# Kernel optimization log

Hardware: AMD Instinct MI355X
Metric: run time of the kernel (lower is better)

## Reference

```python
import jax, jax.numpy as jnp
import numpy as np
from jax import lax

B, L, N = 64, 1024, 64
IN_SZ, MEM_SZ, DEC = 128, 1024, 3


def setup_inputs() -> dict:
    key = jax.random.key(0)
    ks = jax.random.split(key, 8)
    x = jax.random.normal(ks[0], (B, L, N), dtype=jnp.float32)
    # sensor net: Linear(N -> IN_SZ) with bias (stored as [in, out])
    W_sense = jax.random.normal(ks[1], (N, IN_SZ), dtype=jnp.float32) / np.sqrt(N)
    b_sense = jax.random.normal(ks[2], (IN_SZ,), dtype=jnp.float32) * 0.01
    # nBRC: ff_im Linear(IN_SZ -> 3*MEM_SZ, bias=False), ff_mm Linear(MEM_SZ -> 2*MEM_SZ, bias=False)
    W_im = jax.random.normal(ks[3], (IN_SZ, 3 * MEM_SZ), dtype=jnp.float32) / np.sqrt(IN_SZ)
    W_mm = jax.random.normal(ks[4], (MEM_SZ, 2 * MEM_SZ), dtype=jnp.float32) / np.sqrt(MEM_SZ)
    # actor net: Linear(MEM_SZ -> DEC) with bias
    W_act = jax.random.normal(ks[5], (MEM_SZ, DEC), dtype=jnp.float32) / np.sqrt(MEM_SZ)
    b_act = jax.random.normal(ks[6], (DEC,), dtype=jnp.float32) * 0.01
    return {"x": x, "W_sense": W_sense, "b_sense": b_sense,
            "W_im": W_im, "W_mm": W_mm, "W_act": W_act, "b_act": b_act}


def reference(x, W_sense, b_sense, W_im, W_mm, W_act, b_act):
    # sense: applied per-token (flattened in torch; equivalent broadcasted matmul)
    inputs = x @ W_sense + b_sense                      # [B, L, IN_SZ]
    # precompute the input projection for all timesteps in one GEMM
    proj = inputs @ W_im                                 # [B, L, 3*MEM_SZ]
    proj_t = jnp.moveaxis(proj, 1, 0)                    # [L, B, 3*MEM_SZ]
    h0 = jnp.zeros((x.shape[0], MEM_SZ), dtype=x.dtype)

    def step(h, p):
        i_a, i_c, i_o = jnp.split(p, 3, axis=-1)         # each [B, MEM_SZ]
        m = h @ W_mm                                      # [B, 2*MEM_SZ]
        m_a, m_c = jnp.split(m, 2, axis=-1)
        a = 1.0 + jnp.tanh(i_a + m_a)
        c = jax.nn.sigmoid(i_c + m_c)
        hn = c * h + (1.0 - c) * jnp.tanh(i_o + a * h)
        return hn, hn

    _, hs = lax.scan(step, h0, proj_t)                    # [L, B, MEM_SZ]
    memory = jnp.moveaxis(hs, 0, 1)                       # [B, L, MEM_SZ]
    logits = memory @ W_act + b_act                       # [B, L, DEC]
    return jax.nn.softmax(logits, axis=-1)
```

## Files before the change

### kernel.cpp

```cpp
#include <hip/hip_runtime.h>
#include <hip/hip_bf16.h>


#define B_TOT 64
#define L_SEQ 1024
#define N_IN 64
#define INSZ 128
#define MEM 1024
#define DEC 3

#define NGROUP 8
#define BG 8
#define NMEM 32
#define RING 16

typedef __hip_bfloat16 bf16;
typedef short bf16x8 __attribute__((ext_vector_type(8)));
typedef float f32x4 __attribute__((ext_vector_type(4)));
typedef int i32x4 __attribute__((ext_vector_type(4)));
typedef unsigned long long ull;

#define OFF_INPUTS 0
#define SZ_INPUTS  (L_SEQ * 64 * INSZ * 2)
#define OFF_WMM    (OFF_INPUTS + SZ_INPUTS)
#define SZ_WMM     (128 * 32 * 64 * 8 * 2)
#define OFF_WIM    (OFF_WMM + SZ_WMM)
#define SZ_WIM     (192 * 4 * 64 * 8 * 2)
#define OFF_HBUF   (OFF_WIM + SZ_WIM)
#define SZ_HBUF    (RING * NGROUP * BG * MEM * 2)
#define OFF_CTR    (OFF_HBUF + SZ_HBUF)
#define SZ_CTR     ((4096 + 256) * 4)

__device__ __forceinline__ float fast_tanh(float x) {
    float e = __expf(2.f * x);
    return 1.f - 2.f / (e + 1.f);
}
__device__ __forceinline__ float fast_sigmoid(float x) {
    return 1.f / (1.f + __expf(-x));
}

__global__ void k_sense(const float* __restrict__ x, const float* __restrict__ Ws,
                        const float* __restrict__ bs, bf16* __restrict__ inputs) {
    int t = blockIdx.x;
    int tid = threadIdx.x;
    __shared__ float xls[64][64];
    __shared__ float wls[64][128];
    for (int idx = tid; idx < 64 * 64; idx += 256) {
        int b = idx >> 6, k = idx & 63;
        xls[b][k] = x[((size_t)b * L_SEQ + t) * N_IN + k];
    }
    for (int idx = tid; idx < 64 * 128; idx += 256) {
        int k = idx >> 7, j = idx & 127;
        wls[k][j] = Ws[k * INSZ + j];
    }
    __syncthreads();
    int j = tid & 127;
    int bh = tid >> 7;
    float bj = bs[j];
    for (int bi = 0; bi < 32; ++bi) {
        int b = bh * 32 + bi;
        float acc = bj;
#pragma unroll
        for (int k = 0; k < 64; ++k) acc += xls[b][k] * wls[k][j];
        inputs[((size_t)t * 64 + b) * INSZ + j] = (bf16)acc;
    }
}

__global__ void k_pack(const float* __restrict__ Wmm, const float* __restrict__ Wim,
                       bf16* __restrict__ pmm, bf16* __restrict__ pim) {
    int idx = blockIdx.x * 256 + threadIdx.x;
    const int NMMF = 128 * 32 * 64 * 8;
    if (idx < NMMF) {
        int j = idx & 7, lane = (idx >> 3) & 63, kb = (idx >> 9) & 31, ct = idx >> 14;
        int n = ct * 16 + (lane & 15);
        int k = kb * 32 + ((lane >> 4) << 3) + j;
        pmm[idx] = (bf16)Wmm[(size_t)k * 2048 + n];
    } else {
        int idx2 = idx - NMMF;
        if (idx2 < 192 * 4 * 64 * 8) {
            int j = idx2 & 7, lane = (idx2 >> 3) & 63, kb = (idx2 >> 9) & 3, ct = idx2 >> 11;
            int n = ct * 16 + (lane & 15);
            int k = kb * 32 + ((lane >> 4) << 3) + j;
            pim[idx2] = (bf16)Wim[(size_t)k * 3072 + n];
        }
    }
}

__launch_bounds__(256, 1)
__global__ void k_main(const bf16* __restrict__ inputs, const bf16* __restrict__ pmm,
                       const bf16* __restrict__ pim, const float* __restrict__ Wact,
                       const float* __restrict__ bact, bf16* __restrict__ hbuf,
                       float* __restrict__ out, unsigned int* __restrict__ ctr) {
    const int g = blockIdx.x & 7;
    const int m = blockIdx.x >> 3;
    const int tid = (int)threadIdx.x;
    const int wave = tid >> 6;
    const int lane = tid & 63;
    const int r16 = lane & 15;
    const int q = lane >> 4;

    __shared__ float ilds[2][3][2][8][16];
    __shared__ float mpart[2][4][4][8][16];
    __shared__ float wact_lds[3072];
    __shared__ float aplds[2][4][3];
    __shared__ float bactl[3];
    __shared__ unsigned idsl[256];
    __shared__ int fflagl;
    __shared__ float outbuf[L_SEQ * 3];

    for (int idx = tid; idx < 3072; idx += 256) wact_lds[idx] = Wact[idx];
    if (tid < 3) bactl[tid] = bact[tid];

    bf16x8 wb[4][8];
    {
        int base_ct[4] = {2 * m, 2 * m + 1, 64 + 2 * m, 65 + 2 * m};
#pragma unroll
        for (int t4 = 0; t4 < 4; ++t4)
#pragma unroll
            for (int kk = 0; kk < 8; ++kk)
                wb[t4][kk] = *(const bf16x8*)(pmm +
                    (((size_t)base_ct[t4] * 32 + (wave * 8 + kk)) * 64 + lane) * 8);
    }
    bf16x8 wi[2][4];
    if (wave < 3) {
#pragma unroll
        for (int tl = 0; tl < 2; ++tl) {
            int ct2 = wave * 64 + m * 2 + tl;
#pragma unroll
            for (int kb2 = 0; kb2 < 4; ++kb2)
                wi[tl][kb2] = *(const bf16x8*)(pim + (((size_t)ct2 * 4 + kb2) * 64 + lane) * 8);
        }
    }

    f32x4 hreg = {0.f, 0.f, 0.f, 0.f};
    const int erow = lane >> 3;
    const int ec = lane & 7;
    const int ep = ec >> 2;
    const int ecl = (ec & 3) * 4;

    unsigned int* flags = ctr + g * 512;
    unsigned int* ids   = ctr + 4096;

    unsigned xid;
    asm volatile("s_getreg_b32 %0, hwreg(HW_REG_XCC_ID)" : "=s"(xid));
    if (tid == 0)
        __hip_atomic_store(&ids[g * 32 + m], xid + 1u, __ATOMIC_RELAXED,
                           __HIP_MEMORY_SCOPE_AGENT);
    if (wave == 0) {
        int sb = 1 << 20;
        unsigned v0 = 0, v1 = 0, v2 = 0, v3 = 0;
        bool all = false;
        while (!all && --sb > 0) {
            v0 = __hip_atomic_load(&ids[lane], __ATOMIC_RELAXED, __HIP_MEMORY_SCOPE_AGENT);
            v1 = __hip_atomic_load(&ids[64 + lane], __ATOMIC_RELAXED, __HIP_MEMORY_SCOPE_AGENT);
            v2 = __hip_atomic_load(&ids[128 + lane], __ATOMIC_RELAXED, __HIP_MEMORY_SCOPE_AGENT);
            v3 = __hip_atomic_load(&ids[192 + lane], __ATOMIC_RELAXED, __HIP_MEMORY_SCOPE_AGENT);
            all = (bool)__all((int)(v0 && v1 && v2 && v3));
        }
        idsl[lane] = v0; idsl[64 + lane] = v1; idsl[128 + lane] = v2; idsl[192 + lane] = v3;
    }
    __syncthreads();
    if (tid == 0) {
        int f = 1;
        for (int g2 = 0; g2 < 8; ++g2) {
            unsigned r = idsl[g2 * 32];
            for (int k2 = 1; k2 < 32; ++k2) f &= (idsl[g2 * 32 + k2] == r);
        }
        fflagl = f;
    }
    __syncthreads();
    const bool fastf = (fflagl != 0);

    bf16x8 afin[4];
    auto load_in = [&](int t) {
        if (wave < 3) {
            int brow = g * 8 + (r16 & 7);
            const bf16* src = inputs + ((size_t)t * 64 + brow) * INSZ + q * 8;
#pragma unroll
            for (int kb2 = 0; kb2 < 4; ++kb2)
                afin[kb2] = *(const bf16x8*)(src + kb2 * 32);
        }
    };
    auto mma_in_deposit = [&](int t) {
        if (wave < 3) {
            f32x4 a0 = (f32x4){0.f, 0.f, 0.f, 0.f};
            f32x4 a1 = (f32x4){0.f, 0.f, 0.f, 0.f};
#pragma unroll
            for (int kb2 = 0; kb2 < 4; ++kb2) {
                a0 = __builtin_amdgcn_mfma_f32_16x16x32_bf16(afin[kb2], wi[0][kb2], a0, 0, 0, 0);
                a1 = __builtin_amdgcn_mfma_f32_16x16x32_bf16(afin[kb2], wi[1][kb2], a1, 0, 0, 0);
            }
            if (q < 2) {
#pragma unroll
                for (int reg = 0; reg < 4; ++reg) {
                    ilds[t & 1][wave][0][q * 4 + reg][r16] = a0[reg];
                    ilds[t & 1][wave][1][q * 4 + reg][r16] = a1[reg];
                }
            }
        }
    };

    auto poll_own = [&](unsigned target) {
        int k = wave * 8 + (lane & 7);
        bool act = lane < 8;
        unsigned vbest = act ? 0u : target;
        int rounds = 0;
        int sb = 1 << 18;
        while (--sb > 0) {
            if (act && vbest < target) {
                unsigned vm = __hip_atomic_load(&flags[k * 16], __ATOMIC_RELAXED,
                                                __HIP_MEMORY_SCOPE_AGENT);
                if (vm > vbest) vbest = vm;
            }
            if (__all((int)(vbest >= target))) break;
            if (++rounds > 8) __builtin_amdgcn_s_sleep(1);
        }
    };

    auto hload = [&](int t_src, int gg) -> ushort4 {
        int c0 = gg * 4;
        const bf16* hp = hbuf +
            ((size_t)(((t_src & (RING - 1)) * NGROUP + g)) * (BG * MEM)) +
            (c0 >> 5) * 256 + m * 32 + (c0 & 31);
        return *(const ushort4*)hp;
    };
    auto emit_accum = [&](ushort4 hv, int gg, float& p0, float& p1, float& p2) {
        int c0 = gg * 4;
        float h0 = __uint_as_float((unsigned)hv.x << 16);
        float h1 = __uint_as_float((unsigned)hv.y << 16);
        float h2 = __uint_as_float((unsigned)hv.z << 16);
        float h3 = __uint_as_float((unsigned)hv.w << 16);
        const f32x4* wp = (const f32x4*)&wact_lds[c0 * 3];
        f32x4 w0 = wp[0], w1 = wp[1], w2 = wp[2];
        p0 += h0 * w0[0] + h1 * w0[3] + h2 * w1[2] + h3 * w2[1];
        p1 += h0 * w0[1] + h1 * w1[0] + h2 * w1[3] + h3 * w2[2];
        p2 += h0 * w0[2] + h1 * w1[1] + h2 * w2[0] + h3 * w2[3];
    };
    auto emit_reduce = [&](int t_src, float p0, float p1, float p2) {
#pragma unroll
        for (int off = 32; off >= 1; off >>= 1) {
            p0 += __shfl_xor(p0, off);
            p1 += __shfl_xor(p1, off);
            p2 += __shfl_xor(p2, off);
        }
        if (lane == 0) {
            aplds[t_src & 1][wave][0] = p0;
            aplds[t_src & 1][wave][1] = p1;
            aplds[t_src & 1][wave][2] = p2;
        }
    };
    auto fin = [&](int tout) {
        int pr = tout & 1;
        float l0 = aplds[pr][0][0] + aplds[pr][1][0] + aplds[pr][2][0] + bactl[0];
        float l1 = aplds[pr][0][1] + aplds[pr][1][1] + aplds[pr][2][1] + bactl[1];
        float l2 = aplds[pr][0][2] + aplds[pr][1][2] + aplds[pr][2][2] + bactl[2];
        float mx = fmaxf(l0, fmaxf(l1, l2));
        float e0 = __expf(l0 - mx), e1 = __expf(l1 - mx), e2 = __expf(l2 - mx);
        float inv = 1.f / (e0 + e1 + e2);
        outbuf[tout * 3 + 0] = e0 * inv;
        outbuf[tout * 3 + 1] = e1 * inv;
        outbuf[tout * 3 + 2] = e2 * inv;
    };

    auto ew_publish = [&](int t) {
        int par = t & 1;
        f32x4 ma = *(const f32x4*)&mpart[par][0][ep][erow][ecl];
        f32x4 mc = *(const f32x4*)&mpart[par][0][2 + ep][erow][ecl];
#pragma unroll
        for (int w = 1; w < 4; ++w) {
            ma += *(const f32x4*)&mpart[par][w][ep][erow][ecl];
            mc += *(const f32x4*)&mpart[par][w][2 + ep][erow][ecl];
        }
        f32x4 ia = *(const f32x4*)&ilds[par][0][ep][erow][ecl];
        f32x4 ic = *(const f32x4*)&ilds[par][1][ep][erow][ecl];
        f32x4 io = *(const f32x4*)&ilds[par][2][ep][erow][ecl];
        bf16 hb[4];
#pragma unroll
        for (int i = 0; i < 4; ++i) {
            float a = 1.f + fast_tanh(ia[i] + ma[i]);
            float c = fast_sigmoid(ic[i] + mc[i]);
            float hn = c * hreg[i] + (1.f - c) * fast_tanh(io[i] + a * hreg[i]);
            hreg[i] = hn;
            hb[i] = (bf16)hn;
        }
        ull v = *(const ull*)hb;
        bf16* base = hbuf +
            ((size_t)(((t & (RING - 1)) * NGROUP + g)) * (BG * MEM)) + m * 256;
        ull* dst = (ull*)base + lane;
        if (fastf) {
            *dst = v;
        } else {
            __hip_atomic_store(dst, v, __ATOMIC_RELAXED, __HIP_MEMORY_SCOPE_AGENT);
        }
        asm volatile("s_waitcnt vmcnt(0)" ::: "memory");
        if (lane == 0)
            __hip_atomic_store(&flags[m * 16], (unsigned)(t + 1), __ATOMIC_RELAXED,
                               __HIP_MEMORY_SCOPE_AGENT);
    };

    load_in(0);
    mma_in_deposit(0);
    load_in(1);

    ushort4 eh0 = {0, 0, 0, 0}, eh1 = {0, 0, 0, 0};

#pragma clang loop unroll(disable)
    for (int t = 0; t < L_SEQ; ++t) {
        if (t != 0 && (t & (RING - 1)) == 0)
            __builtin_amdgcn_fence(__ATOMIC_ACQUIRE, "agent");

        if (t > 0) poll_own((unsigned)t);

        {
            const bf16* lp = hbuf +
                ((size_t)((((t + RING - 1) & (RING - 1)) * NGROUP + g)) * (BG * MEM)) +
                (size_t)(wave * 8) * 256 + ((r16 & 7) * 32 + q * 8);
            bf16x8 af[8];
#pragma unroll
            for (int kk = 0; kk < 8; ++kk)
                af[kk] = *(const bf16x8*)(lp + kk * 256);
            f32x4 acc0 = {0.f, 0.f, 0.f, 0.f};
            f32x4 acc1 = {0.f, 0.f, 0.f, 0.f};
            f32x4 acc2 = {0.f, 0.f, 0.f, 0.f};
            f32x4 acc3 = {0.f, 0.f, 0.f, 0.f};
#pragma unroll
            for (int kk = 0; kk < 8; ++kk) {
                acc0 = __builtin_amdgcn_mfma_f32_16x16x32_bf16(af[kk], wb[0][kk], acc0, 0, 0, 0);
                acc1 = __builtin_amdgcn_mfma_f32_16x16x32_bf16(af[kk], wb[1][kk], acc1, 0, 0, 0);
                acc2 = __builtin_amdgcn_mfma_f32_16x16x32_bf16(af[kk], wb[2][kk], acc2, 0, 0, 0);
                acc3 = __builtin_amdgcn_mfma_f32_16x16x32_bf16(af[kk], wb[3][kk], acc3, 0, 0, 0);
            }
            if (q < 2) {
                int par = t & 1;
#pragma unroll
                for (int reg = 0; reg < 4; ++reg) {
                    mpart[par][wave][0][q * 4 + reg][r16] = acc0[reg];
                    mpart[par][wave][1][q * 4 + reg][r16] = acc1[reg];
                    mpart[par][wave][2][q * 4 + reg][r16] = acc2[reg];
                    mpart[par][wave][3][q * 4 + reg][r16] = acc3[reg];
                }
            }
        }
        if (m < 8 && t > 0 && wave < 3) eh0 = hload(t - 1, tid);

        asm volatile("s_waitcnt lgkmcnt(0)\n\ts_barrier" ::: "memory");

        if (wave == 3) {
            ew_publish(t);
        } else {
            if (m < 8 && t > 0 && wave == 0) eh1 = hload(t - 1, tid + 192);
            if (t + 1 < L_SEQ) mma_in_deposit(t + 1);
            if (t + 2 < L_SEQ) load_in(t + 2);
            if (m < 8) {
                if (t >= 2 && tid == 64) fin(t - 2);
                if (t > 0) {
                    float p0 = 0.f, p1 = 0.f, p2 = 0.f;
                    emit_accum(eh0, tid, p0, p1, p2);
                    if (wave == 0) emit_accum(eh1, tid + 192, p0, p1, p2);
                    emit_reduce(t - 1, p0, p1, p2);
                }
            }
        }
    }

    if (m < 8) {
        __syncthreads();
        if (tid == 64) fin(L_SEQ - 2);
        poll_own((unsigned)L_SEQ);
        __builtin_amdgcn_fence(__ATOMIC_ACQUIRE, "agent");
        __syncthreads();
        if (wave < 3) {
            float p0 = 0.f, p1 = 0.f, p2 = 0.f;
            ushort4 a = hload(L_SEQ - 1, tid);
            emit_accum(a, tid, p0, p1, p2);
            if (wave == 0) {
                ushort4 b = hload(L_SEQ - 1, tid + 192);
                emit_accum(b, tid + 192, p0, p1, p2);
            }
            emit_reduce(L_SEQ - 1, p0, p1, p2);
        }
        __syncthreads();
        if (tid == 0) fin(L_SEQ - 1);
        __syncthreads();
        float* obase = out + (size_t)(g * 8 + m) * L_SEQ * 3;
        for (int idx = tid; idx < L_SEQ * 3; idx += 256)
            obase[idx] = outbuf[idx];
    }
}

extern "C" void kernel_launch(void* const* d_in, const int* in_sizes, int n_in,
                              void* d_out, int out_size, void* d_ws, size_t ws_size,
                              hipStream_t stream) {
    const float* x    = (const float*)d_in[0];
    const float* Ws   = (const float*)d_in[1];
    const float* bs   = (const float*)d_in[2];
    const float* Wim  = (const float*)d_in[3];
    const float* Wmm  = (const float*)d_in[4];
    const float* Wact = (const float*)d_in[5];
    const float* bact = (const float*)d_in[6];

    char* ws = (char*)d_ws;
    bf16* inputs = (bf16*)(ws + OFF_INPUTS);
    bf16* pmm    = (bf16*)(ws + OFF_WMM);
    bf16* pim    = (bf16*)(ws + OFF_WIM);
    bf16* hbuf   = (bf16*)(ws + OFF_HBUF);
    unsigned int* ctr = (unsigned int*)(ws + OFF_CTR);

    hipMemsetAsync(hbuf, 0, SZ_HBUF, stream);
    hipMemsetAsync(ctr, 0, SZ_CTR, stream);

    k_sense<<<L_SEQ, 256, 0, stream>>>(x, Ws, bs, inputs);
    k_pack<<<(128 * 32 * 64 * 8 + 192 * 4 * 64 * 8) / 256, 256, 0, stream>>>(Wmm, Wim, pmm, pim);
    k_main<<<NGROUP * NMEM, 256, 0, stream>>>(inputs, pmm, pim, Wact, bact, hbuf,
                                              (float*)d_out, ctr);
}
```

Baseline: 2.877 ms.

## Rebalance waves: split recurrent GEMM over three waves, move input projection to wave 3

The K-dimension of the h@W_mm product is now split across waves 0-2 (11/11/10 k-blocks) instead of all four waves taking 8 each. Wave 3 now computes all three gate input projections alongside its elementwise update and publish. The aim is to move the input-projection MFMAs off the critical path of the three GEMM waves and overlap them with the publish on wave 3. In exchange each GEMM wave does more MFMAs and holds more weight registers, and wave 3 takes on extra serial work after publishing, which may lengthen the per-step critical path.

```diff
diff --git a/kernel.cpp b/kernel.cpp
--- a/kernel.cpp
+++ b/kernel.cpp
@@ -99,8 +99,11 @@
     const int r16 = lane & 15;
     const int q = lane >> 4;
 
+    const int mbase = (wave == 0) ? 0 : (wave == 1) ? 11 : 22;
+    const int mcnt  = (wave == 3) ? 0 : ((wave == 2) ? 10 : 11);
+
     __shared__ float ilds[2][3][2][8][16];
-    __shared__ float mpart[2][4][4][8][16];
+    __shared__ float mpart[2][3][4][8][16];
     __shared__ float wact_lds[3072];
     __shared__ float aplds[2][4][3];
     __shared__ float bactl[3];
@@ -111,25 +114,29 @@
     for (int idx = tid; idx < 3072; idx += 256) wact_lds[idx] = Wact[idx];
     if (tid < 3) bactl[tid] = bact[tid];
 
-    bf16x8 wb[4][8];
-    {
+    bf16x8 wb[4][11];
+    if (wave < 3) {
         int base_ct[4] = {2 * m, 2 * m + 1, 64 + 2 * m, 65 + 2 * m};
 #pragma unroll
         for (int t4 = 0; t4 < 4; ++t4)
 #pragma unroll
-            for (int kk = 0; kk < 8; ++kk)
-                wb[t4][kk] = *(const bf16x8*)(pmm +
-                    (((size_t)base_ct[t4] * 32 + (wave * 8 + kk)) * 64 + lane) * 8);
-    }
-    bf16x8 wi[2][4];
-    if (wave < 3) {
-#pragma unroll
-        for (int tl = 0; tl < 2; ++tl) {
-            int ct2 = wave * 64 + m * 2 + tl;
-#pragma unroll
-            for (int kb2 = 0; kb2 < 4; ++kb2)
-                wi[tl][kb2] = *(const bf16x8*)(pim + (((size_t)ct2 * 4 + kb2) * 64 + lane) * 8);
-        }
+            for (int j = 0; j < 11; ++j)
+                if (j < mcnt)
+                    wb[t4][j] = *(const bf16x8*)(pmm +
+                        (((size_t)base_ct[t4] * 32 + (mbase + j)) * 64 + lane) * 8);
+    }
+    bf16x8 wi[3][2][4];
+    if (wave == 3) {
+#pragma unroll
+        for (int gate = 0; gate < 3; ++gate)
+#pragma unroll
+            for (int tl = 0; tl < 2; ++tl) {
+                int ct2 = gate * 64 + m * 2 + tl;
+#pragma unroll
+                for (int kb2 = 0; kb2 < 4; ++kb2)
+                    wi[gate][tl][kb2] = *(const bf16x8*)(pim +
+                        (((size_t)ct2 * 4 + kb2) * 64 + lane) * 8);
+            }
     }
 
     f32x4 hreg = {0.f, 0.f, 0.f, 0.f};
@@ -173,7 +180,7 @@
 
     bf16x8 afin[4];
     auto load_in = [&](int t) {
-        if (wave < 3) {
+        if (wave == 3) {
             int brow = g * 8 + (r16 & 7);
             const bf16* src = inputs + ((size_t)t * 64 + brow) * INSZ + q * 8;
 #pragma unroll
@@ -182,28 +189,31 @@
         }
     };
     auto mma_in_deposit = [&](int t) {
-        if (wave < 3) {
-            f32x4 a0 = (f32x4){0.f, 0.f, 0.f, 0.f};
-            f32x4 a1 = (f32x4){0.f, 0.f, 0.f, 0.f};
-#pragma unroll
-            for (int kb2 = 0; kb2 < 4; ++kb2) {
-                a0 = __builtin_amdgcn_mfma_f32_16x16x32_bf16(afin[kb2], wi[0][kb2], a0, 0, 0, 0);
-                a1 = __builtin_amdgcn_mfma_f32_16x16x32_bf16(afin[kb2], wi[1][kb2], a1, 0, 0, 0);
-            }
-            if (q < 2) {
-#pragma unroll
-                for (int reg = 0; reg < 4; ++reg) {
-                    ilds[t & 1][wave][0][q * 4 + reg][r16] = a0[reg];
-                    ilds[t & 1][wave][1][q * 4 + reg][r16] = a1[reg];
+        if (wave == 3) {
+#pragma unroll
+            for (int gate = 0; gate < 3; ++gate) {
+                f32x4 a0 = (f32x4){0.f, 0.f, 0.f, 0.f};
+                f32x4 a1 = (f32x4){0.f, 0.f, 0.f, 0.f};
+#pragma unroll
+                for (int kb2 = 0; kb2 < 4; ++kb2) {
+                    a0 = __builtin_amdgcn_mfma_f32_16x16x32_bf16(afin[kb2], wi[gate][0][kb2], a0, 0, 0, 0);
+                    a1 = __builtin_amdgcn_mfma_f32_16x16x32_bf16(afin[kb2], wi[gate][1][kb2], a1, 0, 0, 0);
                 }
+                if (q < 2) {
+#pragma unroll
+                    for (int reg = 0; reg < 4; ++reg) {
+                        ilds[t & 1][gate][0][q * 4 + reg][r16] = a0[reg];
+                        ilds[t & 1][gate][1][q * 4 + reg][r16] = a1[reg];
+                    }
+                }
             }
         }
     };
 
     auto poll_own = [&](unsigned target) {
-        int k = wave * 8 + (lane & 7);
-        bool act = lane < 8;
+        bool act = lane < mcnt;
         unsigned vbest = act ? 0u : target;
+        int k = mbase + (act ? lane : 0);
         int rounds = 0;
         int sb = 1 << 18;
         while (--sb > 0) {
@@ -267,7 +277,7 @@
         f32x4 ma = *(const f32x4*)&mpart[par][0][ep][erow][ecl];
         f32x4 mc = *(const f32x4*)&mpart[par][0][2 + ep][erow][ecl];
 #pragma unroll
-        for (int w = 1; w < 4; ++w) {
+        for (int w = 1; w < 3; ++w) {
             ma += *(const f32x4*)&mpart[par][w][ep][erow][ecl];
             mc += *(const f32x4*)&mpart[par][w][2 + ep][erow][ecl];
         }
@@ -309,27 +319,28 @@
         if (t != 0 && (t & (RING - 1)) == 0)
             __builtin_amdgcn_fence(__ATOMIC_ACQUIRE, "agent");
 
-        if (t > 0) poll_own((unsigned)t);
-
-        {
+        if (wave < 3) {
+            if (t > 0) poll_own((unsigned)t);
+
             const bf16* lp = hbuf +
                 ((size_t)((((t + RING - 1) & (RING - 1)) * NGROUP + g)) * (BG * MEM)) +
-                (size_t)(wave * 8) * 256 + ((r16 & 7) * 32 + q * 8);
-            bf16x8 af[8];
-#pragma unroll
-            for (int kk = 0; kk < 8; ++kk)
-                af[kk] = *(const bf16x8*)(lp + kk * 256);
+                (size_t)mbase * 256 + ((r16 & 7) * 32 + q * 8);
+            bf16x8 af[11];
+#pragma unroll
+            for (int j = 0; j < 11; ++j)
+                if (j < mcnt) af[j] = *(const bf16x8*)(lp + j * 256);
             f32x4 acc0 = {0.f, 0.f, 0.f, 0.f};
             f32x4 acc1 = {0.f, 0.f, 0.f, 0.f};
             f32x4 acc2 = {0.f, 0.f, 0.f, 0.f};
             f32x4 acc3 = {0.f, 0.f, 0.f, 0.f};
 #pragma unroll
-            for (int kk = 0; kk < 8; ++kk) {
-                acc0 = __builtin_amdgcn_mfma_f32_16x16x32_bf16(af[kk], wb[0][kk], acc0, 0, 0, 0);
-                acc1 = __builtin_amdgcn_mfma_f32_16x16x32_bf16(af[kk], wb[1][kk], acc1, 0, 0, 0);
-                acc2 = __builtin_amdgcn_mfma_f32_16x16x32_bf16(af[kk], wb[2][kk], acc2, 0, 0, 0);
-                acc3 = __builtin_amdgcn_mfma_f32_16x16x32_bf16(af[kk], wb[3][kk], acc3, 0, 0, 0);
-            }
+            for (int j = 0; j < 11; ++j)
+                if (j < mcnt) {
+                    acc0 = __builtin_amdgcn_mfma_f32_16x16x32_bf16(af[j], wb[0][j], acc0, 0, 0, 0);
+                    acc1 = __builtin_amdgcn_mfma_f32_16x16x32_bf16(af[j], wb[1][j], acc1, 0, 0, 0);
+                    acc2 = __builtin_amdgcn_mfma_f32_16x16x32_bf16(af[j], wb[2][j], acc2, 0, 0, 0);
+                    acc3 = __builtin_amdgcn_mfma_f32_16x16x32_bf16(af[j], wb[3][j], acc3, 0, 0, 0);
+                }
             if (q < 2) {
                 int par = t & 1;
 #pragma unroll
@@ -340,17 +351,17 @@
                     mpart[par][wave][3][q * 4 + reg][r16] = acc3[reg];
                 }
             }
-        }
-        if (m < 8 && t > 0 && wave < 3) eh0 = hload(t - 1, tid);
+            if (m < 8 && t > 0) eh0 = hload(t - 1, tid);
+        }
 
         asm volatile("s_waitcnt lgkmcnt(0)\n\ts_barrier" ::: "memory");
 
         if (wave == 3) {
             ew_publish(t);
+            if (t + 1 < L_SEQ) mma_in_deposit(t + 1);
+            if (t + 2 < L_SEQ) load_in(t + 2);
         } else {
             if (m < 8 && t > 0 && wave == 0) eh1 = hload(t - 1, tid + 192);
-            if (t + 1 < L_SEQ) mma_in_deposit(t + 1);
-            if (t + 2 < L_SEQ) load_in(t + 2);
             if (m < 8) {
                 if (t >= 2 && tid == 64) fin(t - 2);
                 if (t > 0) {
```

Result: slower. 3.331 ms (+15.8%).
